# Optimization experiments

Hardware: AMD Instinct MI355X
Metric: run time of the kernel (lower is better)

Reference implementation:

```python
import jax, jax.numpy as jnp
import numpy as np

DN = ('NCHW', 'OIHW', 'NCHW')

def conv3x3(x, w):
    return jax.lax.conv_general_dilated(x, w, (1, 1), [(1, 1), (1, 1)], dimension_numbers=DN)

def setup_inputs() -> dict:
    key = jax.random.key(0)
    ks = jax.random.split(key, 5)
    N, C, H, W = 64, 512, 16, 16
    fan = C * 3 * 3
    s = 1.0 / np.sqrt(fan)
    x = jax.random.normal(ks[0], (N, C, H, W), dtype=jnp.float32)
    Wq = jax.random.normal(ks[1], (C, C, 3, 3), dtype=jnp.float32) * s
    Wk = jax.random.normal(ks[2], (C, C, 3, 3), dtype=jnp.float32) * s
    Wv = jax.random.normal(ks[3], (C, C, 3, 3), dtype=jnp.float32) * s
    Wc = jax.random.normal(ks[4], (C, C, 3, 3), dtype=jnp.float32) * s
    gamma = jnp.ones((C,), dtype=jnp.float32)
    beta = jnp.zeros((C,), dtype=jnp.float32)
    return {"x": x, "Wq": Wq, "Wk": Wk, "Wv": Wv, "Wc": Wc, "gamma": gamma, "beta": beta}

def reference(x, Wq, Wk, Wv, Wc, gamma, beta):
    C = x.shape[1]
    q = conv3x3(x, Wq)  # [N,C,H,W]
    k = conv3x3(x, Wk)
    v = conv3x3(x, Wv)
    # att[n,m,h,w] = sum_c q[n,c,h,w] * k[m,c,h,w] / sqrt(C); softmax over m
    att = jnp.einsum('nchw,mchw->nmhw', q, k) / jnp.sqrt(jnp.float32(C))
    att = jax.nn.softmax(att, axis=1)
    # virt[n,c,h,w] = sum_m att[n,m,h,w] * v[m,c,h,w]
    virt = jnp.einsum('nmhw,mchw->nchw', att, v)
    # GroupNorm(1, C): normalize over (C,H,W) per sample, per-channel affine
    mu = jnp.mean(virt, axis=(1, 2, 3), keepdims=True)
    var = jnp.var(virt, axis=(1, 2, 3), keepdims=True)
    virt = (virt - mu) * jax.lax.rsqrt(var + 1e-5)
    virt = virt * gamma[None, :, None, None] + beta[None, :, None, None]
    virt = jax.nn.relu(virt)
    virt = conv3x3(virt, Wc)
    # Dropout is identity in eval mode
    return x + virt
```

## Files before the change

kernel.cpp:

```cpp
#include <hip/hip_runtime.h>
#include <math.h>

typedef unsigned short u16;
typedef unsigned int u32;
typedef short short8 __attribute__((ext_vector_type(8)));
typedef float f32x4 __attribute__((ext_vector_type(4)));

#define NB 64
#define CCH 512
#define HW 256

__device__ __forceinline__ u16 f2bf(float f) {
    union { float f; u32 u; } x; x.f = f;
    u32 r = x.u + 0x7fffu + ((x.u >> 16) & 1u);
    return (u16)(r >> 16);
}
__device__ __forceinline__ float bf2f(u16 b) {
    union { u32 u; float f; } x; x.u = ((u32)b) << 16;
    return x.f;
}
__device__ __forceinline__ void gload_lds16(const u16* g, u16* l) {
    __builtin_amdgcn_global_load_lds((const __attribute__((address_space(1))) u32*)g,
                                     (__attribute__((address_space(3))) u32*)l, 16, 0, 0);
}

__global__ __launch_bounds__(256) void zero_borders(u16* __restrict__ pad) {
    const int n = blockIdx.x, t = threadIdx.x;
    short8 z = (short8){0,0,0,0,0,0,0,0};
    for (int idx = t; idx < 68 * 64; idx += 256) {
        int cell = idx >> 6, ch = idx & 63;
        int hh, ww;
        if (cell < 18)      { hh = 0;          ww = cell; }
        else if (cell < 36) { hh = 17;         ww = cell - 18; }
        else if (cell < 52) { hh = cell - 35;  ww = 0; }
        else                { hh = cell - 51;  ww = 17; }
        *(short8*)(pad + ((size_t)((n * 18 + hh) * 18 + ww)) * 512 + ch * 8) = z;
    }
}

__global__ __launch_bounds__(256) void prep_x(const float* __restrict__ x, u16* __restrict__ pad) {
    __shared__ float tl[64][65];
    const int n = blockIdx.z, c0 = blockIdx.y * 64, p0 = blockIdx.x * 64;
    const int t = threadIdx.x;
    {
        const int cc = t >> 2, ps = (t & 3) * 16;
#pragma unroll
        for (int i = 0; i < 4; ++i) {
            float4 v4 = *(const float4*)(x + (((size_t)(n * 512 + c0 + cc)) << 8) + p0 + ps + i * 4);
            tl[cc][ps + i * 4 + 0] = v4.x;
            tl[cc][ps + i * 4 + 1] = v4.y;
            tl[cc][ps + i * 4 + 2] = v4.z;
            tl[cc][ps + i * 4 + 3] = v4.w;
        }
    }
    __syncthreads();
    {
        const int pp = t >> 2, cs = (t & 3) * 16;
        short8 o0, o1;
#pragma unroll
        for (int i = 0; i < 8; ++i) o0[i] = (short)f2bf(tl[cs + i][pp]);
#pragma unroll
        for (int i = 0; i < 8; ++i) o1[i] = (short)f2bf(tl[cs + 8 + i][pp]);
        const int p = p0 + pp, h = p >> 4, wcol = p & 15;
        u16* dst = pad + ((size_t)((n * 18 + h + 1) * 18 + wcol + 1)) * 512 + c0 + cs;
        *(short8*)(dst + 0) = o0;
        *(short8*)(dst + 8) = o1;
    }
}

__global__ __launch_bounds__(256) void prep_w(
    const float* __restrict__ Wq, const float* __restrict__ Wk,
    const float* __restrict__ Wv, const float* __restrict__ Wc,
    u16* __restrict__ Wt)
{
    __shared__ float lw[4608];
    const int co = blockIdx.x, sel = blockIdx.y, t = threadIdx.x;
    const float* Ws = (sel == 0) ? Wq : (sel == 1) ? Wk : (sel == 2) ? Wv : Wc;
#pragma unroll
    for (int i = 0; i < 18; ++i) lw[t + i * 256] = Ws[(size_t)co * 4608 + t + i * 256];
    __syncthreads();
    for (int tap = 0; tap < 9; ++tap)
#pragma unroll
        for (int hh = 0; hh < 2; ++hh) {
            int ci = t + hh * 256;
            Wt[(((size_t)(sel * 9 + tap)) << 18) + (co << 9) + ci] = f2bf(lw[ci * 9 + tap]);
        }
}

__global__ __launch_bounds__(256, 2) void qkv_mfma4(
    const u16* __restrict__ pad, const u16* __restrict__ Wt,
    u16* __restrict__ q, u16* __restrict__ k, u16* __restrict__ v)
{
    __shared__ short As[3][4096];
    __shared__ short Bs[3][6144];
    const int t = threadIdx.x;
    const int l = t & 63;
    const int wid = t >> 6;

    const int o = blockIdx.x;
    const int imbase = (o >> 3) * 128;
    const int cobase = (o & 7) * 192;

    const int cl = ((l & 3) - ((l >> 3) & 3)) & 3;
    int imoffA[2], woffB[3];
#pragma unroll
    for (int rr = 0; rr < 2; ++rr) {
        const int chunk = wid * 2 + rr;
        const int imrow = imbase + chunk * 16 + (l >> 2);
        const int p = imrow >> 6, n = imrow & 63;
        imoffA[rr] = ((n * 18 + (p >> 4)) * 18 + (p & 15)) * 512 + cl * 8;
    }
#pragma unroll
    for (int rr = 0; rr < 3; ++rr) {
        const int cof = cobase + (wid * 3 + rr) * 16 + (l >> 2);
        const int sel = cof >> 9, co = cof & 511;
        woffB[rr] = sel * 9 * 262144 + co * 512 + cl * 8;
    }

    const int fp = ((l >> 4) + (l >> 1)) & 3;
    const int aoff = (l & 15) * 32 + fp * 8;
    const int boff = (wid * 48 + (l & 15)) * 32 + fp * 8;

    f32x4 acc[8][3];
#pragma unroll
    for (int i = 0; i < 8; ++i)
#pragma unroll
        for (int j = 0; j < 3; ++j) acc[i][j] = (f32x4){0.f, 0.f, 0.f, 0.f};

    auto STAGE = [&](int kt, int s) {
        const int tap = kt >> 4;
        const int ashift = ((tap / 3) * 18 + (tap % 3)) * 512 + (kt & 15) * 32;
        const int bshift = tap * 262144 + (kt & 15) * 32;
#pragma unroll
        for (int rr = 0; rr < 2; ++rr)
            gload_lds16(pad + imoffA[rr] + ashift, (u16*)(&As[s][0] + (wid * 2 + rr) * 512));
#pragma unroll
        for (int rr = 0; rr < 3; ++rr)
            gload_lds16(Wt + woffB[rr] + bshift, (u16*)(&Bs[s][0] + (wid * 3 + rr) * 512));
    };

    STAGE(0, 0);
    STAGE(1, 1);

    int s0 = 0;
    short8 fa[8], fb[3];
#pragma unroll 1
    for (int kt = 0; kt < 144; ++kt) {
        const int s2 = (s0 == 0) ? 2 : s0 - 1;
        const short* Ab = &As[s0][0];
        const short* Bb = &Bs[s0][0];

        if (kt >= 143) asm volatile("s_waitcnt vmcnt(0)" ::: "memory");
        else           asm volatile("s_waitcnt vmcnt(5)" ::: "memory");
        __builtin_amdgcn_sched_barrier(0);
        __builtin_amdgcn_s_barrier();
        __builtin_amdgcn_sched_barrier(0);

#pragma unroll
        for (int j = 0; j < 3; ++j) fb[j] = *(const short8*)(Bb + boff + j * 512);
#pragma unroll
        for (int i = 0; i < 8; ++i) fa[i] = *(const short8*)(Ab + aoff + i * 512);

        if (kt < 142) STAGE(kt + 2, s2);

        __builtin_amdgcn_s_setprio(1);
#pragma unroll
        for (int i = 0; i < 8; ++i)
#pragma unroll
            for (int j = 0; j < 3; ++j)
                acc[i][j] = __builtin_amdgcn_mfma_f32_16x16x32_bf16(fa[i], fb[j], acc[i][j], 0, 0, 0);
        __builtin_amdgcn_s_setprio(0);

        s0 = (s0 == 2) ? 0 : s0 + 1;
    }

#pragma unroll
    for (int j = 0; j < 3; ++j) {
        const int colb = cobase + wid * 48 + j * 16;
        u16* op = ((colb >> 9) == 0) ? q : (((colb >> 9) == 1) ? k : v);
        op += (colb & 511) + (l & 15);
#pragma unroll
        for (int i = 0; i < 8; ++i) {
            const int row = imbase + i * 16 + (l >> 4) * 4;
#pragma unroll
            for (int r = 0; r < 4; ++r)
                op[(size_t)(row + r) * 512] = f2bf(acc[i][j][r]);
        }
    }
}

__global__ __launch_bounds__(256, 2) void cres_mfma4(
    const u16* __restrict__ pad, const u16* __restrict__ WtC,
    const float* __restrict__ xres, float* __restrict__ out)
{
    __shared__ short As[3][4096];
    __shared__ short Bs[3][4096];
    const int t = threadIdx.x;
    const int l = t & 63;
    const int wid = t >> 6;
    const int wm = wid >> 1, wn = wid & 1;

    const int o = blockIdx.x;
    const int cobase = (o & 3) * 128;
    const int imbase = (o >> 2) * 128;

    const int cl = ((l & 3) - ((l >> 3) & 3)) & 3;
    int woffA[2], imoffB[2];
#pragma unroll
    for (int rr = 0; rr < 2; ++rr) {
        const int co = cobase + (wid * 2 + rr) * 16 + (l >> 2);
        woffA[rr] = co * 512 + cl * 8;
        const int imrow = imbase + (wid * 2 + rr) * 16 + (l >> 2);
        const int n = imrow >> 8, p = imrow & 255;
        imoffB[rr] = ((n * 18 + (p >> 4)) * 18 + (p & 15)) * 512 + cl * 8;
    }

    const int fp = ((l >> 4) + (l >> 1)) & 3;
    const int aoff = (wm * 64 + (l & 15)) * 32 + fp * 8;
    const int boff = (wn * 64 + (l & 15)) * 32 + fp * 8;

    f32x4 acc[4][4];
#pragma unroll
    for (int i = 0; i < 4; ++i)
#pragma unroll
        for (int j = 0; j < 4; ++j) acc[i][j] = (f32x4){0.f, 0.f, 0.f, 0.f};

    auto STAGE = [&](int kt, int s) {
        const int tap = kt >> 4;
        const int ashift = tap * 262144 + (kt & 15) * 32;
        const int bshift = ((tap / 3) * 18 + (tap % 3)) * 512 + (kt & 15) * 32;
#pragma unroll
        for (int rr = 0; rr < 2; ++rr) {
            gload_lds16(WtC + woffA[rr] + ashift, (u16*)(&As[s][0] + (wid * 2 + rr) * 512));
            gload_lds16(pad + imoffB[rr] + bshift, (u16*)(&Bs[s][0] + (wid * 2 + rr) * 512));
        }
    };

    STAGE(0, 0);
    STAGE(1, 1);

    int s0 = 0;
    short8 fa[4], fb[4];
#pragma unroll 1
    for (int kt = 0; kt < 144; ++kt) {
        const int s2 = (s0 == 0) ? 2 : s0 - 1;
        const short* Ab = &As[s0][0];
        const short* Bb = &Bs[s0][0];

        if (kt >= 143) asm volatile("s_waitcnt vmcnt(0)" ::: "memory");
        else           asm volatile("s_waitcnt vmcnt(4)" ::: "memory");
        __builtin_amdgcn_sched_barrier(0);
        __builtin_amdgcn_s_barrier();
        __builtin_amdgcn_sched_barrier(0);

#pragma unroll
        for (int i = 0; i < 4; ++i) fa[i] = *(const short8*)(Ab + aoff + i * 512);
#pragma unroll
        for (int j = 0; j < 4; ++j) fb[j] = *(const short8*)(Bb + boff + j * 512);

        if (kt < 142) STAGE(kt + 2, s2);

        __builtin_amdgcn_s_setprio(1);
#pragma unroll
        for (int i = 0; i < 4; ++i)
#pragma unroll
            for (int j = 0; j < 4; ++j)
                acc[i][j] = __builtin_amdgcn_mfma_f32_16x16x32_bf16(fa[i], fb[j], acc[i][j], 0, 0, 0);
        __builtin_amdgcn_s_setprio(0);

        s0 = (s0 == 2) ? 0 : s0 + 1;
    }

#pragma unroll
    for (int i = 0; i < 4; ++i)
#pragma unroll
        for (int j = 0; j < 4; ++j)
#pragma unroll
            for (int r = 0; r < 4; ++r) {
                int co = cobase + wm * 64 + i * 16 + (l >> 4) * 4 + r;
                int imrow = imbase + wn * 64 + j * 16 + (l & 15);
                int n = imrow >> 8, p = imrow & 255;
                size_t addr = (((size_t)(n * 512 + co)) << 8) + p;
                out[addr] = acc[i][j][r] + xres[addr];
            }
}

__global__ __launch_bounds__(256) void attn_kernel(
    const u16* __restrict__ qT, const u16* __restrict__ kT, u16* vvT)
{
    const int p = blockIdx.x;
    const int t = threadIdx.x;
    __shared__ float smemA[2][64][68];
    __shared__ float attb[64][68];
    const size_t pb = (size_t)p * (NB * CCH);

    const int ng = t >> 4, mg = t & 15;
    const int n0 = ng * 4, m0 = mg * 4;
    float acc[4][4];
#pragma unroll
    for (int i = 0; i < 4; ++i)
#pragma unroll
        for (int j = 0; j < 4; ++j) acc[i][j] = 0.f;

    for (int ct = 0; ct < 8; ++ct) {
        const int c0 = ct * 64;
        __syncthreads();
#pragma unroll
        for (int s = 0; s < 2; ++s) {
            int f = t + s * 256;
            int nn = f >> 3, c8 = (f & 7) * 8;
            short8 qv = *(const short8*)(qT + pb + (size_t)nn * CCH + c0 + c8);
            short8 kv = *(const short8*)(kT + pb + (size_t)nn * CCH + c0 + c8);
#pragma unroll
            for (int e = 0; e < 8; ++e) {
                smemA[0][nn][c8 + e] = bf2f((u16)qv[e]);
                smemA[1][nn][c8 + e] = bf2f((u16)kv[e]);
            }
        }
        __syncthreads();
#pragma unroll 4
        for (int c4 = 0; c4 < 16; ++c4) {
            float4 q4[4], k4[4];
#pragma unroll
            for (int i = 0; i < 4; ++i) q4[i] = *(const float4*)&smemA[0][n0 + i][c4 * 4];
#pragma unroll
            for (int j = 0; j < 4; ++j) k4[j] = *(const float4*)&smemA[1][m0 + j][c4 * 4];
#pragma unroll
            for (int i = 0; i < 4; ++i)
#pragma unroll
                for (int j = 0; j < 4; ++j) {
                    acc[i][j] = fmaf(q4[i].x, k4[j].x, acc[i][j]);
                    acc[i][j] = fmaf(q4[i].y, k4[j].y, acc[i][j]);
                    acc[i][j] = fmaf(q4[i].z, k4[j].z, acc[i][j]);
                    acc[i][j] = fmaf(q4[i].w, k4[j].w, acc[i][j]);
                }
        }
    }

    const float SCALE = 0.0441941738241592f;
#pragma unroll
    for (int i = 0; i < 4; ++i) {
        float m = fmaxf(fmaxf(acc[i][0], acc[i][1]), fmaxf(acc[i][2], acc[i][3]));
#pragma unroll
        for (int mask = 1; mask < 16; mask <<= 1) m = fmaxf(m, __shfl_xor(m, mask, 16));
        float e[4]; float s = 0.f;
#pragma unroll
        for (int j = 0; j < 4; ++j) { e[j] = __expf((acc[i][j] - m) * SCALE); s += e[j]; }
#pragma unroll
        for (int mask = 1; mask < 16; mask <<= 1) s += __shfl_xor(s, mask, 16);
        float inv = 1.f / s;
#pragma unroll
        for (int j = 0; j < 4; ++j) attb[n0 + i][m0 + j] = e[j] * inv;
    }
    __syncthreads();

    float* vs = &smemA[0][0][0];
    const int ng2 = t >> 3, cg = t & 7;
    const int nn0 = ng2 * 2, cb = cg * 16;
    for (int ct4 = 0; ct4 < 4; ++ct4) {
        const int c0 = ct4 * 128;
#pragma unroll
        for (int s = 0; s < 4; ++s) {
            int f = t + s * 256;
            int m = f >> 4, c8 = (f & 15) * 8;
            short8 vv = *(const short8*)(vvT + pb + (size_t)m * CCH + c0 + c8);
#pragma unroll
            for (int e = 0; e < 8; ++e) vs[m * 132 + c8 + e] = bf2f((u16)vv[e]);
        }
        __syncthreads();
        float acc2[2][16];
#pragma unroll
        for (int i = 0; i < 2; ++i)
#pragma unroll
            for (int j = 0; j < 16; ++j) acc2[i][j] = 0.f;
#pragma unroll 4
        for (int m = 0; m < 64; ++m) {
            float a0 = attb[nn0][m], a1 = attb[nn0 + 1][m];
#pragma unroll
            for (int k4 = 0; k4 < 4; ++k4) {
                float4 v4 = *(const float4*)&vs[m * 132 + cb + k4 * 4];
                acc2[0][k4 * 4 + 0] = fmaf(a0, v4.x, acc2[0][k4 * 4 + 0]);
                acc2[0][k4 * 4 + 1] = fmaf(a0, v4.y, acc2[0][k4 * 4 + 1]);
                acc2[0][k4 * 4 + 2] = fmaf(a0, v4.z, acc2[0][k4 * 4 + 2]);
                acc2[0][k4 * 4 + 3] = fmaf(a0, v4.w, acc2[0][k4 * 4 + 3]);
                acc2[1][k4 * 4 + 0] = fmaf(a1, v4.x, acc2[1][k4 * 4 + 0]);
                acc2[1][k4 * 4 + 1] = fmaf(a1, v4.y, acc2[1][k4 * 4 + 1]);
                acc2[1][k4 * 4 + 2] = fmaf(a1, v4.z, acc2[1][k4 * 4 + 2]);
                acc2[1][k4 * 4 + 3] = fmaf(a1, v4.w, acc2[1][k4 * 4 + 3]);
            }
        }
#pragma unroll
        for (int i = 0; i < 2; ++i)
#pragma unroll
            for (int j = 0; j < 16; ++j)
                vvT[pb + (size_t)(nn0 + i) * CCH + c0 + cb + j] = f2bf(acc2[i][j]);
        __syncthreads();
    }
}

__global__ __launch_bounds__(256) void gn_part1(
    const u16* __restrict__ virtT, float* __restrict__ partials)
{
    const int n = blockIdx.x >> 2, qr = blockIdx.x & 3, t = threadIdx.x;
    float sum = 0.f, ss = 0.f;
#pragma unroll 4
    for (int it = 0; it < 16; ++it) {
        int f = t + it * 256;
        int p = qr * 64 + (f >> 6), c = (f & 63) * 8;
        short8 vv = *(const short8*)(virtT + ((size_t)(p * 64 + n)) * 512 + c);
#pragma unroll
        for (int e = 0; e < 8; ++e) { float x = bf2f((u16)vv[e]); sum += x; ss = fmaf(x, x, ss); }
    }
#pragma unroll
    for (int off = 32; off > 0; off >>= 1) {
        sum += __shfl_down(sum, off);
        ss  += __shfl_down(ss, off);
    }
    __shared__ float rs[4], rss[4];
    const int wid = t >> 6, lane = t & 63;
    if (lane == 0) { rs[wid] = sum; rss[wid] = ss; }
    __syncthreads();
    if (t == 0) {
        partials[(n * 4 + qr) * 2 + 0] = rs[0] + rs[1] + rs[2] + rs[3];
        partials[(n * 4 + qr) * 2 + 1] = rss[0] + rss[1] + rss[2] + rss[3];
    }
}

__global__ __launch_bounds__(256) void gn_part2(
    const u16* __restrict__ virtT, const float* __restrict__ partials,
    const float* __restrict__ gamma, const float* __restrict__ beta,
    u16* __restrict__ ypad)
{
    const int n = blockIdx.x >> 2, qr = blockIdx.x & 3, t = threadIdx.x;
    __shared__ float sg[512], sb[512];
    for (int i = t; i < 512; i += 256) { sg[i] = gamma[i]; sb[i] = beta[i]; }
    float S = 0.f, SS = 0.f;
#pragma unroll
    for (int i = 0; i < 4; ++i) {
        S  += partials[(n * 4 + i) * 2 + 0];
        SS += partials[(n * 4 + i) * 2 + 1];
    }
    const float mu = S * (1.f / 131072.f);
    const float var = SS * (1.f / 131072.f) - mu * mu;
    const float rstd = rsqrtf(var + 1e-5f);
    __syncthreads();

#pragma unroll 4
    for (int it = 0; it < 16; ++it) {
        int f = t + it * 256;
        int p = qr * 64 + (f >> 6), cc = (f & 63) * 8;
        short8 vv = *(const short8*)(virtT + ((size_t)(p * 64 + n)) * 512 + cc);
        short8 ov;
#pragma unroll
        for (int e = 0; e < 8; ++e) {
            float x = (bf2f((u16)vv[e]) - mu) * rstd;
            x = fmaf(x, sg[cc + e], sb[cc + e]);
            ov[e] = (short)f2bf(fmaxf(x, 0.f));
        }
        int h = p >> 4, wcol = p & 15;
        *(short8*)(ypad + ((size_t)((n * 18 + h + 1) * 18 + wcol + 1)) * 512 + cc) = ov;
    }
}

extern "C" void kernel_launch(void* const* d_in, const int* in_sizes, int n_in,
                              void* d_out, int out_size, void* d_ws, size_t ws_size,
                              hipStream_t stream)
{
    const float* x     = (const float*)d_in[0];
    const float* Wq    = (const float*)d_in[1];
    const float* Wk    = (const float*)d_in[2];
    const float* Wv    = (const float*)d_in[3];
    const float* Wc    = (const float*)d_in[4];
    const float* gamma = (const float*)d_in[5];
    const float* beta  = (const float*)d_in[6];
    float* out = (float*)d_out;

    u16* pad = (u16*)d_ws;
    u16* Wt  = pad + 10616832;
    u16* q   = Wt + 9437184;
    u16* k   = q + 8388608;
    u16* v   = k + 8388608;
    float* gnp = (float*)k;

    zero_borders<<<dim3(64), dim3(256), 0, stream>>>(pad);
    prep_x<<<dim3(4, 8, 64), dim3(256), 0, stream>>>(x, pad);
    prep_w<<<dim3(512, 4), dim3(256), 0, stream>>>(Wq, Wk, Wv, Wc, Wt);

    qkv_mfma4<<<dim3(1024), dim3(256), 0, stream>>>(pad, Wt, q, k, v);
    attn_kernel<<<dim3(256), dim3(256), 0, stream>>>(q, k, v);
    gn_part1<<<dim3(256), dim3(256), 0, stream>>>(v, gnp);
    gn_part2<<<dim3(256), dim3(256), 0, stream>>>(v, gnp, gamma, beta, pad);
    cres_mfma4<<<dim3(512), dim3(256), 0, stream>>>(pad, Wt + 3 * 2359296, x, out);
}
```

Before: 436.6 us.

## Retile QKV conv to 512-thread blocks, use MFMA for attention scores, fuse GN stats

The QKV implicit-GEMM conv now uses 512-thread blocks covering a 256x192 output tile, with an 8-wave 2x4 layout and a swizzled block index. Each B weight tile is therefore reused across twice as many image rows. The attention score computation drops the fp32 LDS-based FMA loop and uses bf16 MFMA directly from global memory. The GroupNorm sum and sum-of-squares partials are accumulated in the attention epilogue, which removes the gn_part1 pass that re-read v; the partials buffer moves into the now-unused Q-weight region. The trade-off is lower occupancy (one block per CU) and uneven load issue across waves.

```diff
diff --git a/kernel.cpp b/kernel.cpp
--- a/kernel.cpp
+++ b/kernel.cpp
@@ -87,39 +87,38 @@
         }
 }
 
-__global__ __launch_bounds__(256, 2) void qkv_mfma4(
+__global__ __launch_bounds__(512, 1) void qkv_mfma8(
     const u16* __restrict__ pad, const u16* __restrict__ Wt,
     u16* __restrict__ q, u16* __restrict__ k, u16* __restrict__ v)
 {
-    __shared__ short As[3][4096];
+    __shared__ short As[3][8192];
     __shared__ short Bs[3][6144];
     const int t = threadIdx.x;
     const int l = t & 63;
     const int wid = t >> 6;
+    const int wm = wid >> 2, wn = wid & 3;
 
     const int o = blockIdx.x;
-    const int imbase = (o >> 3) * 128;
-    const int cobase = (o & 7) * 192;
+    const int wg = (o & 7) * 64 + (o >> 3);
+    const int imbase = (wg >> 3) * 256;
+    const int cobase = (wg & 7) * 192;
 
     const int cl = ((l & 3) - ((l >> 3) & 3)) & 3;
-    int imoffA[2], woffB[3];
+    int imoffA[2], woffB[2];
 #pragma unroll
     for (int rr = 0; rr < 2; ++rr) {
         const int chunk = wid * 2 + rr;
         const int imrow = imbase + chunk * 16 + (l >> 2);
         const int p = imrow >> 6, n = imrow & 63;
         imoffA[rr] = ((n * 18 + (p >> 4)) * 18 + (p & 15)) * 512 + cl * 8;
-    }
-#pragma unroll
-    for (int rr = 0; rr < 3; ++rr) {
-        const int cof = cobase + (wid * 3 + rr) * 16 + (l >> 2);
+        const int cof = cobase + chunk * 16 + (l >> 2);
         const int sel = cof >> 9, co = cof & 511;
         woffB[rr] = sel * 9 * 262144 + co * 512 + cl * 8;
     }
 
     const int fp = ((l >> 4) + (l >> 1)) & 3;
-    const int aoff = (l & 15) * 32 + fp * 8;
-    const int boff = (wid * 48 + (l & 15)) * 32 + fp * 8;
+    const int aoff = (wm * 128 + (l & 15)) * 32 + fp * 8;
+    const int boff = (wn * 48 + (l & 15)) * 32 + fp * 8;
 
     f32x4 acc[8][3];
 #pragma unroll
@@ -127,20 +126,25 @@
 #pragma unroll
         for (int j = 0; j < 3; ++j) acc[i][j] = (f32x4){0.f, 0.f, 0.f, 0.f};
 
-    auto STAGE = [&](int kt, int s) {
+    auto STAGE_A = [&](int kt, int s) {
         const int tap = kt >> 4;
-        const int ashift = ((tap / 3) * 18 + (tap % 3)) * 512 + (kt & 15) * 32;
-        const int bshift = tap * 262144 + (kt & 15) * 32;
+        const int shift = ((tap / 3) * 18 + (tap % 3)) * 512 + (kt & 15) * 32;
 #pragma unroll
         for (int rr = 0; rr < 2; ++rr)
-            gload_lds16(pad + imoffA[rr] + ashift, (u16*)(&As[s][0] + (wid * 2 + rr) * 512));
-#pragma unroll
-        for (int rr = 0; rr < 3; ++rr)
-            gload_lds16(Wt + woffB[rr] + bshift, (u16*)(&Bs[s][0] + (wid * 3 + rr) * 512));
+            gload_lds16(pad + imoffA[rr] + shift, (u16*)(&As[s][0] + (wid * 2 + rr) * 512));
     };
-
-    STAGE(0, 0);
-    STAGE(1, 1);
+    auto STAGE_B = [&](int kt, int s) {
+        if (wid < 6) {
+            const int tap = kt >> 4;
+            const int shift = tap * 262144 + (kt & 15) * 32;
+#pragma unroll
+            for (int rr = 0; rr < 2; ++rr)
+                gload_lds16(Wt + woffB[rr] + shift, (u16*)(&Bs[s][0] + (wid * 2 + rr) * 512));
+        }
+    };
+
+    STAGE_A(0, 0); STAGE_B(0, 0);
+    STAGE_A(1, 1); STAGE_B(1, 1);
 
     int s0 = 0;
     short8 fa[8], fb[3];
@@ -150,8 +154,13 @@
         const short* Ab = &As[s0][0];
         const short* Bb = &Bs[s0][0];
 
-        if (kt >= 143) asm volatile("s_waitcnt vmcnt(0)" ::: "memory");
-        else           asm volatile("s_waitcnt vmcnt(5)" ::: "memory");
+        if (kt >= 143) {
+            asm volatile("s_waitcnt vmcnt(0)" ::: "memory");
+        } else if (wid < 6) {
+            asm volatile("s_waitcnt vmcnt(4)" ::: "memory");
+        } else {
+            asm volatile("s_waitcnt vmcnt(2)" ::: "memory");
+        }
         __builtin_amdgcn_sched_barrier(0);
         __builtin_amdgcn_s_barrier();
         __builtin_amdgcn_sched_barrier(0);
@@ -161,7 +170,7 @@
 #pragma unroll
         for (int i = 0; i < 8; ++i) fa[i] = *(const short8*)(Ab + aoff + i * 512);
 
-        if (kt < 142) STAGE(kt + 2, s2);
+        if (kt < 142) { STAGE_A(kt + 2, s2); STAGE_B(kt + 2, s2); }
 
         __builtin_amdgcn_s_setprio(1);
 #pragma unroll
@@ -176,12 +185,12 @@
 
 #pragma unroll
     for (int j = 0; j < 3; ++j) {
-        const int colb = cobase + wid * 48 + j * 16;
+        const int colb = cobase + wn * 48 + j * 16;
         u16* op = ((colb >> 9) == 0) ? q : (((colb >> 9) == 1) ? k : v);
         op += (colb & 511) + (l & 15);
 #pragma unroll
         for (int i = 0; i < 8; ++i) {
-            const int row = imbase + i * 16 + (l >> 4) * 4;
+            const int row = imbase + wm * 128 + i * 16 + (l >> 4) * 4;
 #pragma unroll
             for (int r = 0; r < 4; ++r)
                 op[(size_t)(row + r) * 512] = f2bf(acc[i][j][r]);
@@ -286,82 +295,58 @@
 }
 
 __global__ __launch_bounds__(256) void attn_kernel(
-    const u16* __restrict__ qT, const u16* __restrict__ kT, u16* vvT)
+    const u16* __restrict__ qT, const u16* __restrict__ kT, u16* vvT,
+    float* __restrict__ gnp)
 {
     const int p = blockIdx.x;
     const int t = threadIdx.x;
-    __shared__ float smemA[2][64][68];
+    const int l = t & 63;
+    const int w = t >> 6;
     __shared__ float attb[64][68];
+    __shared__ float vs[8448];
     const size_t pb = (size_t)p * (NB * CCH);
 
-    const int ng = t >> 4, mg = t & 15;
-    const int n0 = ng * 4, m0 = mg * 4;
-    float acc[4][4];
-#pragma unroll
-    for (int i = 0; i < 4; ++i)
-#pragma unroll
-        for (int j = 0; j < 4; ++j) acc[i][j] = 0.f;
-
-    for (int ct = 0; ct < 8; ++ct) {
-        const int c0 = ct * 64;
-        __syncthreads();
-#pragma unroll
-        for (int s = 0; s < 2; ++s) {
-            int f = t + s * 256;
-            int nn = f >> 3, c8 = (f & 7) * 8;
-            short8 qv = *(const short8*)(qT + pb + (size_t)nn * CCH + c0 + c8);
-            short8 kv = *(const short8*)(kT + pb + (size_t)nn * CCH + c0 + c8);
-#pragma unroll
-            for (int e = 0; e < 8; ++e) {
-                smemA[0][nn][c8 + e] = bf2f((u16)qv[e]);
-                smemA[1][nn][c8 + e] = bf2f((u16)kv[e]);
-            }
-        }
-        __syncthreads();
+    const u16* qbase = qT + pb + (size_t)(w * 16 + (l & 15)) * 512 + (l >> 4) * 8;
+    const u16* kbase = kT + pb + (size_t)(l & 15) * 512 + (l >> 4) * 8;
+    f32x4 s[4];
+#pragma unroll
+    for (int j = 0; j < 4; ++j) s[j] = (f32x4){0.f, 0.f, 0.f, 0.f};
 #pragma unroll 4
-        for (int c4 = 0; c4 < 16; ++c4) {
-            float4 q4[4], k4[4];
-#pragma unroll
-            for (int i = 0; i < 4; ++i) q4[i] = *(const float4*)&smemA[0][n0 + i][c4 * 4];
-#pragma unroll
-            for (int j = 0; j < 4; ++j) k4[j] = *(const float4*)&smemA[1][m0 + j][c4 * 4];
-#pragma unroll
-            for (int i = 0; i < 4; ++i)
-#pragma unroll
-                for (int j = 0; j < 4; ++j) {
-                    acc[i][j] = fmaf(q4[i].x, k4[j].x, acc[i][j]);
-                    acc[i][j] = fmaf(q4[i].y, k4[j].y, acc[i][j]);
-                    acc[i][j] = fmaf(q4[i].z, k4[j].z, acc[i][j]);
-                    acc[i][j] = fmaf(q4[i].w, k4[j].w, acc[i][j]);
-                }
+    for (int kc = 0; kc < 16; ++kc) {
+        short8 a = *(const short8*)(qbase + kc * 32);
+#pragma unroll
+        for (int j = 0; j < 4; ++j) {
+            short8 b = *(const short8*)(kbase + (size_t)j * 16 * 512 + kc * 32);
+            s[j] = __builtin_amdgcn_mfma_f32_16x16x32_bf16(a, b, s[j], 0, 0, 0);
         }
     }
 
     const float SCALE = 0.0441941738241592f;
 #pragma unroll
-    for (int i = 0; i < 4; ++i) {
-        float m = fmaxf(fmaxf(acc[i][0], acc[i][1]), fmaxf(acc[i][2], acc[i][3]));
-#pragma unroll
-        for (int mask = 1; mask < 16; mask <<= 1) m = fmaxf(m, __shfl_xor(m, mask, 16));
-        float e[4]; float s = 0.f;
-#pragma unroll
-        for (int j = 0; j < 4; ++j) { e[j] = __expf((acc[i][j] - m) * SCALE); s += e[j]; }
-#pragma unroll
-        for (int mask = 1; mask < 16; mask <<= 1) s += __shfl_xor(s, mask, 16);
-        float inv = 1.f / s;
-#pragma unroll
-        for (int j = 0; j < 4; ++j) attb[n0 + i][m0 + j] = e[j] * inv;
+    for (int r = 0; r < 4; ++r) {
+        float mx = fmaxf(fmaxf(s[0][r], s[1][r]), fmaxf(s[2][r], s[3][r]));
+#pragma unroll
+        for (int mask = 1; mask < 16; mask <<= 1) mx = fmaxf(mx, __shfl_xor(mx, mask));
+        float e[4]; float sm = 0.f;
+#pragma unroll
+        for (int j = 0; j < 4; ++j) { e[j] = __expf((s[j][r] - mx) * SCALE); sm += e[j]; }
+#pragma unroll
+        for (int mask = 1; mask < 16; mask <<= 1) sm += __shfl_xor(sm, mask);
+        float inv = 1.f / sm;
+        const int row = w * 16 + (l >> 4) * 4 + r;
+#pragma unroll
+        for (int j = 0; j < 4; ++j) attb[row][j * 16 + (l & 15)] = e[j] * inv;
     }
     __syncthreads();
 
-    float* vs = &smemA[0][0][0];
     const int ng2 = t >> 3, cg = t & 7;
     const int nn0 = ng2 * 2, cb = cg * 16;
+    float rsum[2] = {0.f, 0.f}, rss[2] = {0.f, 0.f};
     for (int ct4 = 0; ct4 < 4; ++ct4) {
         const int c0 = ct4 * 128;
 #pragma unroll
-        for (int s = 0; s < 4; ++s) {
-            int f = t + s * 256;
+        for (int sld = 0; sld < 4; ++sld) {
+            int f = t + sld * 256;
             int m = f >> 4, c8 = (f & 15) * 8;
             short8 vv = *(const short8*)(vvT + pb + (size_t)m * CCH + c0 + c8);
 #pragma unroll
@@ -392,58 +377,62 @@
 #pragma unroll
         for (int i = 0; i < 2; ++i)
 #pragma unroll
-            for (int j = 0; j < 16; ++j)
-                vvT[pb + (size_t)(nn0 + i) * CCH + c0 + cb + j] = f2bf(acc2[i][j]);
+            for (int j = 0; j < 16; ++j) {
+                float x = acc2[i][j];
+                rsum[i] += x;
+                rss[i] = fmaf(x, x, rss[i]);
+                vvT[pb + (size_t)(nn0 + i) * CCH + c0 + cb + j] = f2bf(x);
+            }
         __syncthreads();
     }
-}
-
-__global__ __launch_bounds__(256) void gn_part1(
-    const u16* __restrict__ virtT, float* __restrict__ partials)
+
+#pragma unroll
+    for (int i = 0; i < 2; ++i) {
+#pragma unroll
+        for (int mask = 1; mask < 8; mask <<= 1) {
+            rsum[i] += __shfl_xor(rsum[i], mask);
+            rss[i]  += __shfl_xor(rss[i],  mask);
+        }
+    }
+    if (cg == 0) {
+#pragma unroll
+        for (int i = 0; i < 2; ++i) {
+            gnp[((size_t)p * 64 + nn0 + i) * 2 + 0] = rsum[i];
+            gnp[((size_t)p * 64 + nn0 + i) * 2 + 1] = rss[i];
+        }
+    }
+}
+
+__global__ __launch_bounds__(256) void gn_part2(
+    const u16* __restrict__ virtT, const float* __restrict__ gnp,
+    const float* __restrict__ gamma, const float* __restrict__ beta,
+    u16* __restrict__ ypad)
 {
     const int n = blockIdx.x >> 2, qr = blockIdx.x & 3, t = threadIdx.x;
-    float sum = 0.f, ss = 0.f;
-#pragma unroll 4
-    for (int it = 0; it < 16; ++it) {
-        int f = t + it * 256;
-        int p = qr * 64 + (f >> 6), c = (f & 63) * 8;
-        short8 vv = *(const short8*)(virtT + ((size_t)(p * 64 + n)) * 512 + c);
-#pragma unroll
-        for (int e = 0; e < 8; ++e) { float x = bf2f((u16)vv[e]); sum += x; ss = fmaf(x, x, ss); }
-    }
+    __shared__ float sg[512], sb[512];
+    for (int i = t; i < 512; i += 256) { sg[i] = gamma[i]; sb[i] = beta[i]; }
+
+    float sum = gnp[((size_t)t * 64 + n) * 2 + 0];
+    float ss  = gnp[((size_t)t * 64 + n) * 2 + 1];
 #pragma unroll
     for (int off = 32; off > 0; off >>= 1) {
         sum += __shfl_down(sum, off);
         ss  += __shfl_down(ss, off);
     }
-    __shared__ float rs[4], rss[4];
+    __shared__ float rs[4], rss[4], stats[2];
     const int wid = t >> 6, lane = t & 63;
     if (lane == 0) { rs[wid] = sum; rss[wid] = ss; }
     __syncthreads();
     if (t == 0) {
-        partials[(n * 4 + qr) * 2 + 0] = rs[0] + rs[1] + rs[2] + rs[3];
-        partials[(n * 4 + qr) * 2 + 1] = rss[0] + rss[1] + rss[2] + rss[3];
-    }
-}
-
-__global__ __launch_bounds__(256) void gn_part2(
-    const u16* __restrict__ virtT, const float* __restrict__ partials,
-    const float* __restrict__ gamma, const float* __restrict__ beta,
-    u16* __restrict__ ypad)
-{
-    const int n = blockIdx.x >> 2, qr = blockIdx.x & 3, t = threadIdx.x;
-    __shared__ float sg[512], sb[512];
-    for (int i = t; i < 512; i += 256) { sg[i] = gamma[i]; sb[i] = beta[i]; }
-    float S = 0.f, SS = 0.f;
-#pragma unroll
-    for (int i = 0; i < 4; ++i) {
-        S  += partials[(n * 4 + i) * 2 + 0];
-        SS += partials[(n * 4 + i) * 2 + 1];
-    }
-    const float mu = S * (1.f / 131072.f);
-    const float var = SS * (1.f / 131072.f) - mu * mu;
-    const float rstd = rsqrtf(var + 1e-5f);
+        float S = rs[0] + rs[1] + rs[2] + rs[3];
+        float SS = rss[0] + rss[1] + rss[2] + rss[3];
+        float mu = S * (1.f / 131072.f);
+        float var = SS * (1.f / 131072.f) - mu * mu;
+        stats[0] = mu;
+        stats[1] = rsqrtf(var + 1e-5f);
+    }
     __syncthreads();
+    const float mu = stats[0], rstd = stats[1];
 
 #pragma unroll 4
     for (int it = 0; it < 16; ++it) {
@@ -480,15 +469,14 @@
     u16* q   = Wt + 9437184;
     u16* k   = q + 8388608;
     u16* v   = k + 8388608;
-    float* gnp = (float*)k;
+    float* gnp = (float*)Wt;
 
     zero_borders<<<dim3(64), dim3(256), 0, stream>>>(pad);
     prep_x<<<dim3(4, 8, 64), dim3(256), 0, stream>>>(x, pad);
     prep_w<<<dim3(512, 4), dim3(256), 0, stream>>>(Wq, Wk, Wv, Wc, Wt);
 
-    qkv_mfma4<<<dim3(1024), dim3(256), 0, stream>>>(pad, Wt, q, k, v);
-    attn_kernel<<<dim3(256), dim3(256), 0, stream>>>(q, k, v);
-    gn_part1<<<dim3(256), dim3(256), 0, stream>>>(v, gnp);
+    qkv_mfma8<<<dim3(512), dim3(512), 0, stream>>>(pad, Wt, q, k, v);
+    attn_kernel<<<dim3(256), dim3(256), 0, stream>>>(q, k, v, gnp);
     gn_part2<<<dim3(256), dim3(256), 0, stream>>>(v, gnp, gamma, beta, pad);
     cres_mfma4<<<dim3(512), dim3(256), 0, stream>>>(pad, Wt + 3 * 2359296, x, out);
 }
```

Result: faster. 391.0 us (-10.4%).
